# Optimization experiments

Hardware: AMD Instinct MI355X
Metric: run time of the kernel (lower is better)

Reference implementation:

```python
import jax, jax.numpy as jnp
from jax import lax
import numpy as np

B, HW = 256, 64          # batch, image side (grayscale)
L, E, K = 32, 64, 8192   # latent_size, embedding_size, num_embeddings
DN = ('NHWC', 'HWIO', 'NHWC')


def setup_inputs() -> dict:
    key = jax.random.key(0)
    ks = jax.random.split(key, 21)
    n = lambda k, shape, s=0.05: (jax.random.normal(k, shape, jnp.float32) * s)
    return {
        'x': jax.random.uniform(ks[0], (B, HW, HW), jnp.float32),
        # encoder convs (SAME, stride 2): 64->32->16->8
        'enc_w1': n(ks[1], (4, 4, 1, 32)),   'enc_b1': jnp.zeros((32,), jnp.float32),
        'enc_w2': n(ks[2], (4, 4, 32, 64)),  'enc_b2': jnp.zeros((64,), jnp.float32),
        'enc_w3': n(ks[3], (4, 4, 64, 128)), 'enc_b3': jnp.zeros((128,), jnp.float32),
        # encoder dense: flatten 8*8*128=8192 -> 512 -> L*E=2048
        'fc_w': n(ks[4], (8192, 512), 0.02), 'fc_b': jnp.zeros((512,), jnp.float32),
        'ffc_w': n(ks[5], (512, L * E), 0.02), 'ffc_b': jnp.zeros((L * E,), jnp.float32),
        # VQ codebook
        'embeds': n(ks[6], (K, E), 0.02),
        # decoder dense: 2048 -> 512, then 1x1x512 feature map
        'dec_fc_w': n(ks[7], (L * E, 512), 0.02), 'dec_fc_b': jnp.zeros((512,), jnp.float32),
        # decoder conv_transpose VALID: 1->4->16->64
        'dec_w1': n(ks[8], (4, 4, 512, 256)),  'dec_b1': jnp.zeros((256,), jnp.float32),
        'dec_w2': n(ks[9], (4, 4, 256, 128)),  'dec_b2': jnp.zeros((128,), jnp.float32),
        'dec_w3': n(ks[10], (4, 4, 128, 1)),   'dec_b3': jnp.zeros((1,), jnp.float32),
    }


def _conv(h, w, b, s):
    return jax.nn.relu(lax.conv_general_dilated(h, w, (s, s), 'SAME', dimension_numbers=DN) + b)


def reference(x, enc_w1, enc_b1, enc_w2, enc_b2, enc_w3, enc_b3,
              fc_w, fc_b, ffc_w, ffc_b, embeds,
              dec_fc_w, dec_fc_b, dec_w1, dec_b1, dec_w2, dec_b2, dec_w3, dec_b3):
    # ---- encoder ----
    h = x[..., None]                                   # (B,64,64,1)
    h = _conv(h, enc_w1, enc_b1, 2)                    # (B,32,32,32)
    h = _conv(h, enc_w2, enc_b2, 2)                    # (B,16,16,64)
    h = _conv(h, enc_w3, enc_b3, 2)                    # (B,8,8,128)
    h = h.reshape(h.shape[0], -1)                      # (B,8192)
    h = jax.nn.relu(h @ fc_w + fc_b)                   # (B,512)
    pred = jax.nn.relu(h @ ffc_w + ffc_b).reshape(-1, L, E)  # (B,L,E)
    # ---- VQ middle: nearest codebook entry (argmin of L2 norm == argmin of squared dist) ----
    d2 = (jnp.sum(pred * pred, axis=-1, keepdims=True)
          - 2.0 * jnp.einsum('ble,ke->blk', pred, embeds)
          + jnp.sum(embeds * embeds, axis=-1))         # (B,L,K)
    classes = jnp.argmin(d2, axis=-1)                  # (B,L) int
    collected = embeds[classes]                        # (B,L,E) gather
    h = collected.reshape(-1, L * E)                   # (B,2048)
    # ---- decoder ----
    h = jax.nn.relu(h @ dec_fc_w + dec_fc_b)           # (B,512)
    h = h[:, None, None, :]                            # (B,1,1,512)
    h = jax.nn.relu(lax.conv_transpose(h, dec_w1, (1, 1), 'VALID', dimension_numbers=DN) + dec_b1)  # (B,4,4,256)
    h = jax.nn.relu(lax.conv_transpose(h, dec_w2, (4, 4), 'VALID', dimension_numbers=DN) + dec_b2)  # (B,16,16,128)
    out = lax.conv_transpose(h, dec_w3, (4, 4), 'VALID', dimension_numbers=DN) + dec_b3             # (B,64,64,1)
    return out  # L2 loss_type: output_t = logits_t
```

## Files before the change

### kernel.cpp

```cpp
#include <hip/hip_runtime.h>
#include <cfloat>


typedef short bf16x8 __attribute__((ext_vector_type(8)));
typedef float f32x4 __attribute__((ext_vector_type(4)));
#define MFMA16(a, b, c) __builtin_amdgcn_mfma_f32_16x16x32_bf16(a, b, c, 0, 0, 0)

__device__ inline unsigned short f2bf(float x) {
  unsigned u = __float_as_uint(x);
  u += 0x7fffu + ((u >> 16) & 1u);
  return (unsigned short)(u >> 16);
}
__device__ inline float bf2f(unsigned short h) {
  return __uint_as_float(((unsigned)h) << 16);
}
__device__ inline void split3v(float v, unsigned short& hb, unsigned short& mb,
                               unsigned short& lb) {
  hb = f2bf(v);
  float r1 = v - bf2f(hb);
  mb = f2bf(r1);
  lb = f2bf(r1 - bf2f(mb));
}

#define PB0 12672
#define PB1 (PB0 + 13056)
#define PB2 (PB1 + 128)
#define PB3 (PB2 + 512)
#define PB4 (PB3 + 2048)
#define PB5 (PB4 + 32)
#define PB6 (PB5 + 4096)
#define PB7 (PB6 + 2048)
__global__ __launch_bounds__(256) void k_prep_early(
    const float* __restrict__ enc_w2, const float* __restrict__ enc_w3,
    const float* __restrict__ embeds, const float* __restrict__ dec_fc_w,
    const float* __restrict__ dec_w2, unsigned short* __restrict__ h1base,
    unsigned short* __restrict__ h2base, unsigned short* __restrict__ Wp2H,
    unsigned short* __restrict__ Wp2M, unsigned short* __restrict__ Wp2L,
    unsigned short* __restrict__ Wp3H, unsigned short* __restrict__ Wp3M,
    unsigned short* __restrict__ Wp3L, unsigned short* __restrict__ eB,
    float* __restrict__ n2, unsigned short* __restrict__ Bp_dfc,
    unsigned short* __restrict__ Bp_d2) {
  int blk = blockIdx.x;
  int t = threadIdx.x;
  if (blk < PB0) {
    int li = blk * 256 + t;
    int bc = li & 8191;
    int rest = li >> 13;
    int i = rest % 132, plane = rest / 132;
    int b = bc >> 5, c = bc & 31;
    int row, col;
    if (i < 34) { row = 0; col = i; }
    else if (i < 68) { row = 33; col = i - 34; }
    else { int j = i - 68; row = 1 + (j >> 1); col = (j & 1) ? 33 : 0; }
    h1base[(size_t)plane * 9469952 + ((size_t)(b * 34 + row) * 34 + col) * 32 + c] = 0;
  } else if (blk < PB1) {
    int li = (blk - PB0) * 256 + t;
    int bc = li & 16383;
    int rest = li >> 14;
    int i = rest % 68, plane = rest / 68;
    int b = bc >> 6, c = bc & 63;
    int row, col;
    if (i < 18) { row = 0; col = i; }
    else if (i < 36) { row = 17; col = i - 18; }
    else { int j = i - 36; row = 1 + (j >> 1); col = (j & 1) ? 17 : 0; }
    h2base[(size_t)plane * 5308416 + ((size_t)(b * 18 + row) * 18 + col) * 64 + c] = 0;
  } else if (blk < PB2) {
    int idx = (blk - PB1) * 256 + t;
    int j = idx & 7, lane = (idx >> 3) & 63, nt = (idx >> 9) & 3, s = idx >> 11;
    int ci = ((lane >> 4) << 3) + j, co = (nt << 4) + (lane & 15);
    unsigned short hb, mb, lb;
    split3v(enc_w2[(s * 32 + ci) * 64 + co], hb, mb, lb);
    Wp2H[idx] = hb; Wp2M[idx] = mb; Wp2L[idx] = lb;
  } else if (blk < PB3) {
    int idx = (blk - PB2) * 256 + t;
    int j = idx & 7, lane = (idx >> 3) & 63, ks = (idx >> 9) & 1;
    int nt = (idx >> 10) & 3, ch = (idx >> 12) & 1, s = idx >> 13;
    int ci = ks * 32 + ((lane >> 4) << 3) + j;
    int co = ch * 64 + (nt << 4) + (lane & 15);
    unsigned short hb, mb, lb;
    split3v(enc_w3[(s * 64 + ci) * 128 + co], hb, mb, lb);
    Wp3H[idx] = hb; Wp3M[idx] = mb; Wp3L[idx] = lb;
  } else if (blk < PB4) {
    int idx = (blk - PB3) * 256 + t;
    int j = idx & 7, lane = (idx >> 3) & 63;
    int f = idx >> 9;
    int nt = f & 3, ks = (f >> 2) & 1, kt = f >> 3;
    int code = kt * 64 + nt * 16 + (lane & 15);
    int k = ks * 32 + ((lane >> 4) << 3) + j;
    unsigned short hb, mb, lb;
    split3v(embeds[(size_t)code * 64 + k], hb, mb, lb);
    size_t base = (size_t)f * 1536 + lane * 8 + j;
    eB[base] = hb; eB[base + 512] = mb; eB[base + 1024] = lb;
  } else if (blk < PB5) {
    int k = (blk - PB4) * 256 + t;
    const float4* p = (const float4*)(embeds + (size_t)k * 64);
    float s0 = 0, s1 = 0, s2 = 0, s3 = 0;
#pragma unroll
    for (int j = 0; j < 16; ++j) {
      float4 v = p[j];
      s0 = fmaf(v.x, v.x, s0); s1 = fmaf(v.y, v.y, s1);
      s2 = fmaf(v.z, v.z, s2); s3 = fmaf(v.w, v.w, s3);
    }
    n2[k] = (s0 + s1) + (s2 + s3);
  } else if (blk < PB6) {
    int idx = (blk - PB5) * 256 + t;
    int j = idx & 7, lane = (idx >> 3) & 63;
    int f = idx >> 9;
    int ntg = f & 31;
    int kt = f >> 5;
    int k = kt * 32 + ((lane >> 4) << 3) + j;
    int n = ntg * 16 + (lane & 15);
    unsigned short hb, mb, lb;
    split3v(dec_fc_w[(size_t)k * 512 + n], hb, mb, lb);
    Bp_dfc[idx] = hb; Bp_dfc[idx + 1048576] = mb;
  } else if (blk < PB7) {
    int idx = (blk - PB6) * 256 + t;
    int j = idx & 7, lane = (idx >> 3) & 63;
    int f = idx >> 9;
    int ntg = f & 127;
    int kt = f >> 7;
    int k = kt * 32 + ((lane >> 4) << 3) + j;
    int n = ntg * 16 + (lane & 15);
    int o = n & 127, ru = n >> 7;
    int r = ru >> 2, u = ru & 3;
    int sf = (3 - r) * 4 + (3 - u);
    unsigned short hb, mb, lb;
    split3v(dec_w2[(((size_t)sf * 256 + k) << 7) + o], hb, mb, lb);
    Bp_d2[idx] = hb; Bp_d2[idx + 524288] = mb;
  }
}

__global__ __launch_bounds__(256) void k_conv1(const float* __restrict__ x,
                                               const float* __restrict__ w,
                                               const float* __restrict__ bias,
                                               unsigned short* __restrict__ oH,
                                               unsigned short* __restrict__ oM,
                                               unsigned short* __restrict__ oL) {
  int b = blockIdx.x >> 5;
  int y = blockIdx.x & 31;
  int t = threadIdx.x;
  int c = t & 31;
  int xg = t >> 5;
  float acc[4] = {0.f, 0.f, 0.f, 0.f};
  for (int dy = 0; dy < 4; ++dy) {
    int iy = 2 * y + dy - 1;
    if (iy < 0 || iy >= 64) continue;
    const float* xrow = x + ((size_t)b * 64 + iy) * 64;
    for (int dx = 0; dx < 4; ++dx) {
      float wv = w[(dy * 4 + dx) * 32 + c];
#pragma unroll
      for (int i = 0; i < 4; ++i) {
        int ix = 8 * xg + 2 * i + dx - 1;
        float v = (ix >= 0 && ix < 64) ? xrow[ix] : 0.f;
        acc[i] = fmaf(v, wv, acc[i]);
      }
    }
  }
  float bv = bias[c];
#pragma unroll
  for (int i = 0; i < 4; ++i) {
    float v = acc[i] + bv;
    v = v > 0.f ? v : 0.f;
    unsigned short hb, mb, lb;
    split3v(v, hb, mb, lb);
    size_t o = ((size_t)(b * 34 + y + 1) * 34 + (4 * xg + i + 1)) * 32 + c;
    oH[o] = hb; oM[o] = mb; oL[o] = lb;
  }
}

__global__ __launch_bounds__(1024, 4) void k_conv2s(
    const unsigned short* __restrict__ aH, const unsigned short* __restrict__ aM,
    const unsigned short* __restrict__ aL, const unsigned short* __restrict__ wH,
    const unsigned short* __restrict__ wM, const unsigned short* __restrict__ wL,
    const float* __restrict__ bias, unsigned short* __restrict__ oH,
    unsigned short* __restrict__ oM, unsigned short* __restrict__ oL) {
  __shared__ unsigned short Bs[49152];
  int t = threadIdx.x;
  int wave = t >> 6, lane = t & 63;
  int l15 = lane & 15, quad = lane >> 4;
  int m0 = blockIdx.x * 256 + wave * 16;
  int p = m0 + l15;
  int b = p >> 8, y = (p >> 4) & 15, x = p & 15;
  f32x4 acc[4] = {};
#pragma unroll
  for (int hf = 0; hf < 2; ++hf) {
    if (hf) __syncthreads();
    {
      const unsigned short* s0 = wH + hf * 16384;
      const unsigned short* s1 = wM + hf * 16384;
      const unsigned short* s2 = wL + hf * 16384;
#pragma unroll
      for (int i = 0; i < 2; ++i) {
        int o8 = (i * 1024 + t) * 8;
        *(bf16x8*)(Bs + o8)         = *(const bf16x8*)(s0 + o8);
        *(bf16x8*)(Bs + 16384 + o8) = *(const bf16x8*)(s1 + o8);
        *(bf16x8*)(Bs + 32768 + o8) = *(const bf16x8*)(s2 + o8);
      }
    }
    __syncthreads();
#pragma unroll 4
    for (int sl = 0; sl < 8; ++sl) {
      int s = hf * 8 + sl;
      int dy = s >> 2, dx = s & 3;
      size_t aoff = ((size_t)(b * 34 + 2 * y + dy) * 34 + (2 * x + dx)) * 32 + quad * 8;
      bf16x8 ah = *(const bf16x8*)(aH + aoff);
      bf16x8 am = *(const bf16x8*)(aM + aoff);
      bf16x8 al = *(const bf16x8*)(aL + aoff);
#pragma unroll
      for (int nt = 0; nt < 4; ++nt) {
        const unsigned short* bp = Bs + ((sl * 4 + nt) * 64 + lane) * 8;
        bf16x8 bh = *(const bf16x8*)(bp);
        bf16x8 bm = *(const bf16x8*)(bp + 16384);
        bf16x8 bl = *(const bf16x8*)(bp + 32768);
        acc[nt] = MFMA16(am, bm, acc[nt]);
        acc[nt] = MFMA16(ah, bl, acc[nt]);
        acc[nt] = MFMA16(al, bh, acc[nt]);
        acc[nt] = MFMA16(ah, bm, acc[nt]);
        acc[nt] = MFMA16(am, bh, acc[nt]);
        acc[nt] = MFMA16(ah, bh, acc[nt]);
      }
    }
  }
#pragma unroll
  for (int r = 0; r < 4; ++r) {
    int pp = m0 + quad * 4 + r;
    int b2 = pp >> 8, yo = (pp >> 4) & 15, xo = pp & 15;
    size_t obase = ((size_t)(b2 * 18 + yo + 1) * 18 + (xo + 1)) * 64;
#pragma unroll
    for (int nt = 0; nt < 4; ++nt) {
      int co = nt * 16 + l15;
      float v = acc[nt][r] + bias[co];
      v = v > 0.f ? v : 0.f;
      unsigned short hb, mb, lb;
      split3v(v, hb, mb, lb);
      oH[obase + co] = hb; oM[obase + co] = mb; oL[obase + co] = lb;
    }
  }
}

__global__ __launch_bounds__(256, 4) void k_conv3m(
    const unsigned short* __restrict__ aH, const unsigned short* __restrict__ aM,
    const unsigned short* __restrict__ aL, const unsigned short* __restrict__ wH,
    const unsigned short* __restrict__ wM, const unsigned short* __restrict__ wL,
    float* __restrict__ part) {
  int t = threadIdx.x;
  int wave = t >> 6, lane = t & 63;
  int l15 = lane & 15, quad = lane >> 4;
  int mtg = wave & 1, ch = wave >> 1;
  int m0 = blockIdx.x * 32 + mtg * 16;
  int z = blockIdx.y;
  int p = m0 + l15;
  int b = p >> 6, y = (p >> 3) & 7, x = p & 7;
  f32x4 acc[4] = {};
#pragma unroll 2
  for (int si = 0; si < 8; ++si) {
    int s = z * 8 + si;
    int dy = s >> 2, dx = s & 3;
    size_t base = ((size_t)(b * 18 + 2 * y + dy) * 18 + (2 * x + dx)) * 64 + quad * 8;
    bf16x8 ah[2], am[2], al[2];
#pragma unroll
    for (int ks = 0; ks < 2; ++ks) {
      ah[ks] = *(const bf16x8*)(aH + base + ks * 32);
      am[ks] = *(const bf16x8*)(aM + base + ks * 32);
      al[ks] = *(const bf16x8*)(aL + base + ks * 32);
    }
#pragma unroll
    for (int nt = 0; nt < 4; ++nt) {
#pragma unroll
      for (int ks = 0; ks < 2; ++ks) {
        size_t woff = ((size_t)((((s * 2 + ch) * 4 + nt) * 2 + ks) * 64 + lane)) * 8;
        bf16x8 bh = *(const bf16x8*)(wH + woff);
        bf16x8 bm = *(const bf16x8*)(wM + woff);
        bf16x8 bl = *(const bf16x8*)(wL + woff);
        acc[nt] = MFMA16(am[ks], bm, acc[nt]);
        acc[nt] = MFMA16(ah[ks], bl, acc[nt]);
        acc[nt] = MFMA16(al[ks], bh, acc[nt]);
        acc[nt] = MFMA16(ah[ks], bm, acc[nt]);
        acc[nt] = MFMA16(am[ks], bh, acc[nt]);
        acc[nt] = MFMA16(ah[ks], bh, acc[nt]);
      }
    }
  }
  float* Cp = part + (size_t)z * 2097152;
#pragma unroll
  for (int nt = 0; nt < 4; ++nt) {
    int co = ch * 64 + nt * 16 + l15;
#pragma unroll
    for (int r = 0; r < 4; ++r) {
      int pp = m0 + quad * 4 + r;
      Cp[(size_t)pp * 128 + co] = acc[nt][r];
    }
  }
}

#define FB0 8192
#define FB1 (FB0 + 16384)
__global__ __launch_bounds__(256) void k_prep_fc(
    const float* __restrict__ part, const float* __restrict__ enc_b3,
    unsigned short* __restrict__ h3H, unsigned short* __restrict__ h3M,
    unsigned short* __restrict__ h3L, const float* __restrict__ fc_w,
    unsigned short* __restrict__ Bp_fc) {
  int blk = blockIdx.x;
  int t = threadIdx.x;
  if (blk < FB0) {
    int idx = blk * 256 + t;
    float s = part[idx] + part[2097152 + idx] + enc_b3[idx & 127];
    s = s > 0.f ? s : 0.f;
    unsigned short hb, mb, lb;
    split3v(s, hb, mb, lb);
    h3H[idx] = hb; h3M[idx] = mb; h3L[idx] = lb;
  } else {
    int idx = (blk - FB0) * 256 + t;
    int j = idx & 7, lane = (idx >> 3) & 63;
    int f = idx >> 9;
    int ntg = f & 31;
    int kt = f >> 5;
    int k = kt * 32 + ((lane >> 4) << 3) + j;
    int n = ntg * 16 + (lane & 15);
    unsigned short hb, mb, lb;
    split3v(fc_w[(size_t)k * 512 + n], hb, mb, lb);
    Bp_fc[idx] = hb; Bp_fc[idx + 4194304] = mb; Bp_fc[idx + 8388608] = lb;
  }
}

#define WB0 4096
#define WB1 (WB0 + 8192)
__global__ __launch_bounds__(256) void k_prep_w2(
    const float* __restrict__ ffc_w, unsigned short* __restrict__ Bp_ffc,
    const float* __restrict__ dec_w1, unsigned short* __restrict__ Bp_d1) {
  int blk = blockIdx.x;
  int t = threadIdx.x;
  if (blk < WB0) {
    int idx = blk * 256 + t;
    int j = idx & 7, lane = (idx >> 3) & 63;
    int f = idx >> 9;
    int ntg = f & 127;
    int kt = f >> 7;
    int k = kt * 32 + ((lane >> 4) << 3) + j;
    int n = ntg * 16 + (lane & 15);
    unsigned short hb, mb, lb;
    split3v(ffc_w[(size_t)k * 2048 + n], hb, mb, lb);
    Bp_ffc[idx] = hb; Bp_ffc[idx + 1048576] = mb; Bp_ffc[idx + 2097152] = lb;
  } else {
    int idx = (blk - WB0) * 256 + t;
    int j = idx & 7, lane = (idx >> 3) & 63;
    int f = idx >> 9;
    int ntg = f & 255;
    int kt = f >> 8;
    int k = kt * 32 + ((lane >> 4) << 3) + j;
    int n = ntg * 16 + (lane & 15);
    int o = n & 255, ru = n >> 8;
    int r = ru >> 2, u = ru & 3;
    int sf = (3 - r) * 4 + (3 - u);
    unsigned short hb, mb, lb;
    split3v(dec_w1[(((size_t)sf * 512 + k) << 8) + o], hb, mb, lb);
    Bp_d1[idx] = hb; Bp_d1[idx + 2097152] = mb;
  }
}

template <int NP, int NTW>
__global__ __launch_bounds__(256) void k_mgemm(
    const unsigned short* __restrict__ A0, const unsigned short* __restrict__ A1,
    const unsigned short* __restrict__ A2, const unsigned short* __restrict__ Bp,
    float* __restrict__ C, const float* __restrict__ bias,
    int M, int N, int K, int bmask) {
  int S = gridDim.z;
  int Kc = K / S;
  int t = threadIdx.x;
  int wave = t >> 6, lane = t & 63;
  int l15 = lane & 15, quad = lane >> 4;
  int m0 = blockIdx.x * 64 + wave * 16;
  int n0 = blockIdx.y * (16 * NTW);
  int KT = K >> 5, NT = N >> 4;
  int kt0 = (blockIdx.z * Kc) >> 5;
  int ktn = Kc >> 5;
  size_t sstride = (size_t)KT * NT * 512;
  const unsigned short* arow0 = A0 + (size_t)(m0 + l15) * K + quad * 8;
  const unsigned short* arow1 = A1 + (size_t)(m0 + l15) * K + quad * 8;
  const unsigned short* arow2 = nullptr;
  if constexpr (NP == 3) arow2 = A2 + (size_t)(m0 + l15) * K + quad * 8;
  f32x4 acc[NTW] = {};
  for (int kt = kt0; kt < kt0 + ktn; ++kt) {
    bf16x8 ah = *(const bf16x8*)(arow0 + kt * 32);
    bf16x8 am = *(const bf16x8*)(arow1 + kt * 32);
    bf16x8 al;
    if constexpr (NP == 3) al = *(const bf16x8*)(arow2 + kt * 32);
    const unsigned short* bbase =
        Bp + ((size_t)kt * NT + (n0 >> 4)) * 512 + lane * 8;
#pragma unroll
    for (int nt = 0; nt < NTW; ++nt) {
      const unsigned short* bp = bbase + nt * 512;
      bf16x8 bh = *(const bf16x8*)(bp);
      bf16x8 bm = *(const bf16x8*)(bp + sstride);
      if constexpr (NP == 3) {
        bf16x8 bl = *(const bf16x8*)(bp + 2 * sstride);
        acc[nt] = MFMA16(am, bm, acc[nt]);
        acc[nt] = MFMA16(ah, bl, acc[nt]);
        acc[nt] = MFMA16(al, bh, acc[nt]);
        acc[nt] = MFMA16(ah, bm, acc[nt]);
        acc[nt] = MFMA16(am, bh, acc[nt]);
        acc[nt] = MFMA16(ah, bh, acc[nt]);
      } else {
        acc[nt] = MFMA16(ah, bm, acc[nt]);
        acc[nt] = MFMA16(am, bh, acc[nt]);
        acc[nt] = MFMA16(ah, bh, acc[nt]);
      }
    }
  }
  if (S == 1) {
#pragma unroll
    for (int nt = 0; nt < NTW; ++nt) {
      int n = n0 + nt * 16 + l15;
      float bv = bias[n & bmask];
#pragma unroll
      for (int r = 0; r < 4; ++r) {
        int m = m0 + quad * 4 + r;
        float v = acc[nt][r] + bv;
        C[(size_t)m * N + n] = v > 0.f ? v : 0.f;
      }
    }
  } else {
    float* Cp = C + (size_t)blockIdx.z * M * N;
#pragma unroll
    for (int nt = 0; nt < NTW; ++nt) {
      int n = n0 + nt * 16 + l15;
#pragma unroll
      for (int r = 0; r < 4; ++r) {
        int m = m0 + quad * 4 + r;
        Cp[(size_t)m * N + n] = acc[nt][r];
      }
    }
  }
}

template <int NPOUT>
__global__ __launch_bounds__(256) void k_sumrelu3(
    const float* __restrict__ part, const float* __restrict__ bias,
    unsigned short* __restrict__ oH, unsigned short* __restrict__ oM,
    unsigned short* __restrict__ oL, int MN, int bmask, int S) {
  int idx = blockIdx.x * 256 + threadIdx.x;
  float s = 0.f;
  for (int z = 0; z < S; ++z) s += part[(size_t)z * MN + idx];
  s += bias[idx & bmask];
  s = s > 0.f ? s : 0.f;
  unsigned short hb = f2bf(s);
  float r1 = s - bf2f(hb);
  unsigned short mb = f2bf(r1);
  oH[idx] = hb; oM[idx] = mb;
  if constexpr (NPOUT == 3) oL[idx] = f2bf(r1 - bf2f(mb));
}

__global__ __launch_bounds__(256) void k_vqmfma3(
    const unsigned short* __restrict__ pH, const unsigned short* __restrict__ pM,
    const unsigned short* __restrict__ pL, const unsigned short* __restrict__ eB,
    const float* __restrict__ n2, float* __restrict__ pbd, int* __restrict__ pbk) {
  int t = threadIdx.x;
  int wave = t >> 6, lane = t & 63;
  int l15 = lane & 15, quad = lane >> 4;
  int m0 = blockIdx.x * 128 + wave * 32;
  int z = blockIdx.y;
  bf16x8 ah[2][2], am[2][2], al[2][2];
#pragma unroll
  for (int mt = 0; mt < 2; ++mt) {
    size_t arow = (size_t)(m0 + mt * 16 + l15) * 64 + quad * 8;
#pragma unroll
    for (int ks = 0; ks < 2; ++ks) {
      ah[mt][ks] = *(const bf16x8*)(pH + arow + ks * 32);
      am[mt][ks] = *(const bf16x8*)(pM + arow + ks * 32);
      al[mt][ks] = *(const bf16x8*)(pL + arow + ks * 32);
    }
  }
  float bd[2][4]; int bk[2][4];
#pragma unroll
  for (int mt = 0; mt < 2; ++mt)
#pragma unroll
    for (int r = 0; r < 4; ++r) { bd[mt][r] = FLT_MAX; bk[mt][r] = 0; }
  for (int kt = z * 16; kt < z * 16 + 16; ++kt) {
    const unsigned short* bb = eB + (size_t)kt * 12288 + lane * 8;
    f32x4 acc[2][4] = {};
#pragma unroll
    for (int ks = 0; ks < 2; ++ks)
#pragma unroll
      for (int nt = 0; nt < 4; ++nt) {
        const unsigned short* bp = bb + ((ks * 4 + nt) * 3) * 512;
        bf16x8 bh = *(const bf16x8*)(bp);
        bf16x8 bm = *(const bf16x8*)(bp + 512);
        bf16x8 bl = *(const bf16x8*)(bp + 1024);
#pragma unroll
        for (int mt = 0; mt < 2; ++mt) {
          acc[mt][nt] = MFMA16(am[mt][ks], bm, acc[mt][nt]);
          acc[mt][nt] = MFMA16(ah[mt][ks], bl, acc[mt][nt]);
          acc[mt][nt] = MFMA16(al[mt][ks], bh, acc[mt][nt]);
          acc[mt][nt] = MFMA16(ah[mt][ks], bm, acc[mt][nt]);
          acc[mt][nt] = MFMA16(am[mt][ks], bh, acc[mt][nt]);
          acc[mt][nt] = MFMA16(ah[mt][ks], bh, acc[mt][nt]);
        }
      }
    int cb = kt * 64;
#pragma unroll
    for (int nt = 0; nt < 4; ++nt) {
      int code = cb + nt * 16 + l15;
      float nv = n2[code];
#pragma unroll
      for (int mt = 0; mt < 2; ++mt)
#pragma unroll
        for (int r = 0; r < 4; ++r) {
          float d = fmaf(-2.f, acc[mt][nt][r], nv);
          if (d < bd[mt][r]) { bd[mt][r] = d; bk[mt][r] = code; }
        }
    }
  }
#pragma unroll
  for (int mt = 0; mt < 2; ++mt)
#pragma unroll
    for (int r = 0; r < 4; ++r)
#pragma unroll
      for (int s = 1; s < 16; s <<= 1) {
        float od = __shfl_xor(bd[mt][r], s);
        int ok = __shfl_xor(bk[mt][r], s);
        if (od < bd[mt][r] || (od == bd[mt][r] && ok < bk[mt][r])) {
          bd[mt][r] = od; bk[mt][r] = ok;
        }
      }
  if (l15 == 0) {
#pragma unroll
    for (int mt = 0; mt < 2; ++mt)
#pragma unroll
      for (int r = 0; r < 4; ++r) {
        pbd[(size_t)z * 8192 + m0 + mt * 16 + quad * 4 + r] = bd[mt][r];
        pbk[(size_t)z * 8192 + m0 + mt * 16 + quad * 4 + r] = bk[mt][r];
      }
  }
}

__global__ __launch_bounds__(256) void k_vqgather(const float* __restrict__ pbd,
                                                  const int* __restrict__ pbk,
                                                  const float* __restrict__ embeds,
                                                  unsigned short* __restrict__ cH,
                                                  unsigned short* __restrict__ cM) {
  int idx = blockIdx.x * 256 + threadIdx.x;
  int m = idx >> 6;
  float bd = pbd[m]; int bk = pbk[m];
#pragma unroll
  for (int z = 1; z < 8; ++z) {
    float d = pbd[(size_t)z * 8192 + m]; int k = pbk[(size_t)z * 8192 + m];
    if (d < bd || (d == bd && k < bk)) { bd = d; bk = k; }
  }
  float v = embeds[(size_t)bk * 64 + (idx & 63)];
  unsigned short hb = f2bf(v);
  cH[idx] = hb;
  cM[idx] = f2bf(v - bf2f(hb));
}

__global__ __launch_bounds__(256) void k_dec3(const float* __restrict__ d2buf,
                                              const float* __restrict__ w3,
                                              const float* __restrict__ b3,
                                              float* __restrict__ out) {
  __shared__ float sx[16 * 129];
  __shared__ float wT[128 * 16];
  int b = blockIdx.x >> 4;
  int y = blockIdx.x & 15;
  int t = threadIdx.x;
#pragma unroll
  for (int j = 0; j < 8; ++j) {
    int idx = t + j * 256;
    int xx = idx >> 7, c = idx & 127;
    size_t m2 = ((size_t)b * 4 + (y >> 2)) * 4 + (xx >> 2);
    sx[xx * 129 + c] = d2buf[m2 * 2048 + ((y & 3) * 4 + (xx & 3)) * 128 + c];
  }
#pragma unroll
  for (int j = 0; j < 8; ++j) {
    int idx = t + j * 256;
    int c = idx >> 4, ru = idx & 15;
    int R = ru >> 2, U = ru & 3;
    wT[c * 16 + ru] = w3[((3 - R) * 4 + (3 - U)) * 128 + c];
  }
  __syncthreads();
  int xx = t >> 4, ru = t & 15;
  float a0 = 0, a1 = 0, a2 = 0, a3 = 0;
#pragma unroll 8
  for (int c = 0; c < 128; c += 4) {
    a0 = fmaf(sx[xx * 129 + c + 0], wT[(c + 0) * 16 + ru], a0);
    a1 = fmaf(sx[xx * 129 + c + 1], wT[(c + 1) * 16 + ru], a1);
    a2 = fmaf(sx[xx * 129 + c + 2], wT[(c + 2) * 16 + ru], a2);
    a3 = fmaf(sx[xx * 129 + c + 3], wT[(c + 3) * 16 + ru], a3);
  }
  float acc = (a0 + a1) + (a2 + a3) + b3[0];
  int R = ru >> 2, U = ru & 3;
  out[((size_t)b * 64 + 4 * y + R) * 64 + 4 * xx + U] = acc;
}

extern "C" void kernel_launch(void* const* d_in, const int* in_sizes, int n_in,
                              void* d_out, int out_size, void* d_ws, size_t ws_size,
                              hipStream_t stream) {
  const float* x        = (const float*)d_in[0];
  const float* enc_w1   = (const float*)d_in[1];
  const float* enc_b1   = (const float*)d_in[2];
  const float* enc_w2   = (const float*)d_in[3];
  const float* enc_b2   = (const float*)d_in[4];
  const float* enc_w3   = (const float*)d_in[5];
  const float* enc_b3   = (const float*)d_in[6];
  const float* fc_w     = (const float*)d_in[7];
  const float* fc_b     = (const float*)d_in[8];
  const float* ffc_w    = (const float*)d_in[9];
  const float* ffc_b    = (const float*)d_in[10];
  const float* embeds   = (const float*)d_in[11];
  const float* dec_fc_w = (const float*)d_in[12];
  const float* dec_fc_b = (const float*)d_in[13];
  const float* dec_w1   = (const float*)d_in[14];
  const float* dec_b1   = (const float*)d_in[15];
  const float* dec_w2   = (const float*)d_in[16];
  const float* dec_b2   = (const float*)d_in[17];
  const float* dec_w3   = (const float*)d_in[18];
  const float* dec_b3   = (const float*)d_in[19];
  float* outp = (float*)d_out;

  char* ws = (char*)d_ws;
  size_t off = 0;
  auto alloc = [&](size_t bytes) { size_t r = off; off = (off + bytes + 255) & ~(size_t)255; return r; };

  size_t RA = alloc(57147392);
  unsigned short* h1pH = (unsigned short*)(ws + RA);
  unsigned short* h1pM = (unsigned short*)(ws + RA + 18939904);
  unsigned short* h1pL = (unsigned short*)(ws + RA + 37879808);
  float* d2buf            = (float*)(ws + RA);
  float* partials         = (float*)(ws + RA + 33554432);
  unsigned short* Bp_d1   = (unsigned short*)(ws + RA + 41943040);
  unsigned short* d1H     = (unsigned short*)(ws + RA + 50331648);
  unsigned short* d1M     = (unsigned short*)(ws + RA + 52428800);
  unsigned short* hdH     = (unsigned short*)(ws + RA + 54525952);
  unsigned short* hdM     = (unsigned short*)(ws + RA + 54788096);
  unsigned short* cH      = (unsigned short*)(ws + RA + 55050240);
  unsigned short* cM      = (unsigned short*)(ws + RA + 56098816);

  size_t RB = alloc(31850496);
  unsigned short* h2pH = (unsigned short*)(ws + RB);
  unsigned short* h2pM = (unsigned short*)(ws + RB + 10616832);
  unsigned short* h2pL = (unsigned short*)(ws + RB + 21233664);
  unsigned short* Bp_fc = (unsigned short*)(ws + RB);
  unsigned short* pH    = (unsigned short*)(ws + RB + 28311552);
  unsigned short* pM    = (unsigned short*)(ws + RB + 29360128);
  unsigned short* pL    = (unsigned short*)(ws + RB + 30408704);

  size_t RC = alloc(12582912);
  unsigned short* h3H = (unsigned short*)(ws + RC);
  unsigned short* h3M = (unsigned short*)(ws + RC + 4194304);
  unsigned short* h3L = (unsigned short*)(ws + RC + 8388608);
  unsigned short* Bp_ffc = (unsigned short*)(ws + RC);
  unsigned short* hfcH   = (unsigned short*)(ws + RC + 6291456);
  unsigned short* hfcM   = (unsigned short*)(ws + RC + 6553600);
  unsigned short* hfcL   = (unsigned short*)(ws + RC + 6815744);

  unsigned short* eB     = (unsigned short*)(ws + alloc(3145728));
  unsigned short* Bp_dfc = (unsigned short*)(ws + alloc(4194304));
  unsigned short* Bp_d2  = (unsigned short*)(ws + alloc(2097152));
  float* n2buf   = (float*)(ws + alloc(32768));
  float* pbd     = (float*)(ws + alloc(262144));
  int*   pbk     = (int*)  (ws + alloc(262144));
  unsigned short* Wp2H = (unsigned short*)(ws + alloc(196608));
  unsigned short* Wp2M = Wp2H + 32768;
  unsigned short* Wp2L = Wp2M + 32768;
  unsigned short* Wp3H = (unsigned short*)(ws + alloc(786432));
  unsigned short* Wp3M = Wp3H + 131072;
  unsigned short* Wp3L = Wp3M + 131072;
  (void)ws_size; (void)in_sizes; (void)n_in; (void)out_size;

  k_prep_early<<<PB7, 256, 0, stream>>>(
      enc_w2, enc_w3, embeds, dec_fc_w, dec_w2, h1pH, h2pH,
      Wp2H, Wp2M, Wp2L, Wp3H, Wp3M, Wp3L, eB, n2buf, Bp_dfc, Bp_d2);

  k_conv1<<<8192, 256, 0, stream>>>(x, enc_w1, enc_b1, h1pH, h1pM, h1pL);
  k_conv2s<<<256, 1024, 0, stream>>>(h1pH, h1pM, h1pL, Wp2H, Wp2M, Wp2L,
                                     enc_b2, h2pH, h2pM, h2pL);
  k_conv3m<<<dim3(512, 2), 256, 0, stream>>>(h2pH, h2pM, h2pL,
                                             Wp3H, Wp3M, Wp3L, partials);
  k_prep_fc<<<FB1, 256, 0, stream>>>(partials, enc_b3, h3H, h3M, h3L,
                                     fc_w, Bp_fc);

  k_mgemm<3, 4><<<dim3(4, 8, 16), 256, 0, stream>>>(
      h3H, h3M, h3L, Bp_fc, partials, fc_b, 256, 512, 8192, 511);
  k_prep_w2<<<WB1, 256, 0, stream>>>(ffc_w, Bp_ffc, dec_w1, Bp_d1);
  k_sumrelu3<3><<<512, 256, 0, stream>>>(partials, fc_b, hfcH, hfcM, hfcL,
                                         131072, 511, 16);
  k_mgemm<3, 4><<<dim3(4, 32, 4), 256, 0, stream>>>(
      hfcH, hfcM, hfcL, Bp_ffc, partials, ffc_b, 256, 2048, 512, 2047);
  k_sumrelu3<3><<<2048, 256, 0, stream>>>(partials, ffc_b, pH, pM, pL,
                                          524288, 2047, 4);

  k_vqmfma3<<<dim3(64, 8), 256, 0, stream>>>(pH, pM, pL, eB, n2buf, pbd, pbk);
  k_vqgather<<<2048, 256, 0, stream>>>(pbd, pbk, embeds, cH, cM);

  k_mgemm<2, 4><<<dim3(4, 8, 16), 256, 0, stream>>>(
      cH, cM, nullptr, Bp_dfc, partials, dec_fc_b, 256, 512, 2048, 511);
  k_sumrelu3<2><<<512, 256, 0, stream>>>(partials, dec_fc_b, hdH, hdM, nullptr,
                                         131072, 511, 16);

  k_mgemm<2, 4><<<dim3(4, 64, 2), 256, 0, stream>>>(
      hdH, hdM, nullptr, Bp_d1, partials, dec_b1, 256, 4096, 512, 255);
  k_sumrelu3<2><<<4096, 256, 0, stream>>>(partials, dec_b1, d1H, d1M, nullptr,
                                          1048576, 255, 2);

  k_mgemm<2, 8><<<dim3(64, 16, 1), 256, 0, stream>>>(
      d1H, d1M, nullptr, Bp_d2, d2buf, dec_b2, 4096, 2048, 256, 127);

  k_dec3<<<4096, 256, 0, stream>>>(d2buf, dec_w3, dec_b3, outp);
}
```

Baseline: 444.5 us.

## Stage conv3 weights in double-buffered LDS and enlarge per-wave M tile

The third encoder conv kernel now stages each tap's packed hi/mid/lo weight slices in shared memory with a register-staged double buffer, so weights are no longer re-read from global memory by every wave. Each wave also covers two 16-row M tiles per B fragment, and the block grows to 512 threads handling 128 output pixels. This removes redundant global weight traffic and reuses each B load across more MFMAs. In exchange it uses 96KB of LDS per block, adds a barrier per tap, raises register pressure and launches fewer blocks (256 instead of 1024).

```diff
diff --git a/kernel.cpp b/kernel.cpp
--- a/kernel.cpp
+++ b/kernel.cpp
@@ -238,59 +238,105 @@
   }
 }
 
-__global__ __launch_bounds__(256, 4) void k_conv3m(
+__global__ __launch_bounds__(512, 2) void k_conv3s(
     const unsigned short* __restrict__ aH, const unsigned short* __restrict__ aM,
     const unsigned short* __restrict__ aL, const unsigned short* __restrict__ wH,
     const unsigned short* __restrict__ wM, const unsigned short* __restrict__ wL,
     float* __restrict__ part) {
+  __shared__ unsigned short Bs[2][24576];
   int t = threadIdx.x;
   int wave = t >> 6, lane = t & 63;
   int l15 = lane & 15, quad = lane >> 4;
-  int mtg = wave & 1, ch = wave >> 1;
-  int m0 = blockIdx.x * 32 + mtg * 16;
+  int ch = wave & 1, mg = wave >> 1;
+  int m0 = blockIdx.x * 128 + mg * 32;
   int z = blockIdx.y;
-  int p = m0 + l15;
-  int b = p >> 6, y = (p >> 3) & 7, x = p & 7;
-  f32x4 acc[4] = {};
+  f32x4 acc[2][4] = {};
+  {
+    const unsigned short* srcH = wH + (size_t)(z * 8) * 8192;
+    const unsigned short* srcM = wM + (size_t)(z * 8) * 8192;
+    const unsigned short* srcL = wL + (size_t)(z * 8) * 8192;
+#pragma unroll
+    for (int i = 0; i < 2; ++i) {
+      int o8 = (i * 512 + t) * 8;
+      *(bf16x8*)(&Bs[0][o8])         = *(const bf16x8*)(srcH + o8);
+      *(bf16x8*)(&Bs[0][8192 + o8])  = *(const bf16x8*)(srcM + o8);
+      *(bf16x8*)(&Bs[0][16384 + o8]) = *(const bf16x8*)(srcL + o8);
+    }
+  }
+  __syncthreads();
 #pragma unroll 2
   for (int si = 0; si < 8; ++si) {
     int s = z * 8 + si;
+    int cur = si & 1, nxt = cur ^ 1;
+    bf16x8 stg[6];
+    if (si < 7) {
+      const unsigned short* srcH = wH + (size_t)(s + 1) * 8192;
+      const unsigned short* srcM = wM + (size_t)(s + 1) * 8192;
+      const unsigned short* srcL = wL + (size_t)(s + 1) * 8192;
+#pragma unroll
+      for (int i = 0; i < 2; ++i) {
+        int o8 = (i * 512 + t) * 8;
+        stg[i]     = *(const bf16x8*)(srcH + o8);
+        stg[2 + i] = *(const bf16x8*)(srcM + o8);
+        stg[4 + i] = *(const bf16x8*)(srcL + o8);
+      }
+    }
     int dy = s >> 2, dx = s & 3;
-    size_t base = ((size_t)(b * 18 + 2 * y + dy) * 18 + (2 * x + dx)) * 64 + quad * 8;
-    bf16x8 ah[2], am[2], al[2];
-#pragma unroll
-    for (int ks = 0; ks < 2; ++ks) {
-      ah[ks] = *(const bf16x8*)(aH + base + ks * 32);
-      am[ks] = *(const bf16x8*)(aM + base + ks * 32);
-      al[ks] = *(const bf16x8*)(aL + base + ks * 32);
-    }
+    bf16x8 ah[2][2], am[2][2], al[2][2];
+#pragma unroll
+    for (int mt = 0; mt < 2; ++mt) {
+      int p = m0 + mt * 16 + l15;
+      int b = p >> 6, y = (p >> 3) & 7, x = p & 7;
+      size_t base = ((size_t)(b * 18 + 2 * y + dy) * 18 + (2 * x + dx)) * 64 + quad * 8;
+#pragma unroll
+      for (int ks = 0; ks < 2; ++ks) {
+        ah[mt][ks] = *(const bf16x8*)(aH + base + ks * 32);
+        am[mt][ks] = *(const bf16x8*)(aM + base + ks * 32);
+        al[mt][ks] = *(const bf16x8*)(aL + base + ks * 32);
+      }
+    }
+#pragma unroll
+    for (int nt = 0; nt < 4; ++nt)
+#pragma unroll
+      for (int ks = 0; ks < 2; ++ks) {
+        const unsigned short* bp =
+            &Bs[cur][((ch * 4 + nt) * 2 + ks) * 512 + lane * 8];
+        bf16x8 bh = *(const bf16x8*)(bp);
+        bf16x8 bm = *(const bf16x8*)(bp + 8192);
+        bf16x8 bl = *(const bf16x8*)(bp + 16384);
+#pragma unroll
+        for (int mt = 0; mt < 2; ++mt) {
+          acc[mt][nt] = MFMA16(am[mt][ks], bm, acc[mt][nt]);
+          acc[mt][nt] = MFMA16(ah[mt][ks], bl, acc[mt][nt]);
+          acc[mt][nt] = MFMA16(al[mt][ks], bh, acc[mt][nt]);
+          acc[mt][nt] = MFMA16(ah[mt][ks], bm, acc[mt][nt]);
+          acc[mt][nt] = MFMA16(am[mt][ks], bh, acc[mt][nt]);
+          acc[mt][nt] = MFMA16(ah[mt][ks], bh, acc[mt][nt]);
+        }
+      }
+    if (si < 7) {
+#pragma unroll
+      for (int i = 0; i < 2; ++i) {
+        int o8 = (i * 512 + t) * 8;
+        *(bf16x8*)(&Bs[nxt][o8])         = stg[i];
+        *(bf16x8*)(&Bs[nxt][8192 + o8])  = stg[2 + i];
+        *(bf16x8*)(&Bs[nxt][16384 + o8]) = stg[4 + i];
+      }
+    }
+    __syncthreads();
+  }
+  float* Cp = part + (size_t)z * 2097152;
+#pragma unroll
+  for (int mt = 0; mt < 2; ++mt)
 #pragma unroll
     for (int nt = 0; nt < 4; ++nt) {
-#pragma unroll
-      for (int ks = 0; ks < 2; ++ks) {
-        size_t woff = ((size_t)((((s * 2 + ch) * 4 + nt) * 2 + ks) * 64 + lane)) * 8;
-        bf16x8 bh = *(const bf16x8*)(wH + woff);
-        bf16x8 bm = *(const bf16x8*)(wM + woff);
-        bf16x8 bl = *(const bf16x8*)(wL + woff);
-        acc[nt] = MFMA16(am[ks], bm, acc[nt]);
-        acc[nt] = MFMA16(ah[ks], bl, acc[nt]);
-        acc[nt] = MFMA16(al[ks], bh, acc[nt]);
-        acc[nt] = MFMA16(ah[ks], bm, acc[nt]);
-        acc[nt] = MFMA16(am[ks], bh, acc[nt]);
-        acc[nt] = MFMA16(ah[ks], bh, acc[nt]);
-      }
-    }
-  }
-  float* Cp = part + (size_t)z * 2097152;
-#pragma unroll
-  for (int nt = 0; nt < 4; ++nt) {
-    int co = ch * 64 + nt * 16 + l15;
-#pragma unroll
-    for (int r = 0; r < 4; ++r) {
-      int pp = m0 + quad * 4 + r;
-      Cp[(size_t)pp * 128 + co] = acc[nt][r];
-    }
-  }
+      int co = ch * 64 + nt * 16 + l15;
+#pragma unroll
+      for (int r = 0; r < 4; ++r) {
+        int pp = m0 + mt * 16 + quad * 4 + r;
+        Cp[(size_t)pp * 128 + co] = acc[mt][nt][r];
+      }
+    }
 }
 
 #define FB0 8192
@@ -672,7 +718,7 @@
   k_conv1<<<8192, 256, 0, stream>>>(x, enc_w1, enc_b1, h1pH, h1pM, h1pL);
   k_conv2s<<<256, 1024, 0, stream>>>(h1pH, h1pM, h1pL, Wp2H, Wp2M, Wp2L,
                                      enc_b2, h2pH, h2pM, h2pL);
-  k_conv3m<<<dim3(512, 2), 256, 0, stream>>>(h2pH, h2pM, h2pL,
+  k_conv3s<<<dim3(128, 2), 512, 0, stream>>>(h2pH, h2pM, h2pL,
                                              Wp3H, Wp3M, Wp3L, partials);
   k_prep_fc<<<FB1, 256, 0, stream>>>(partials, enc_b3, h3H, h3M, h3L,
                                      fc_w, Bp_fc);
```

Result: faster. 431.8 us (-2.9%).
